# Kernel tuning notes

Hardware: AMD Instinct MI355X
Metric: run time of the kernel (lower is better)

## Reference

```python
import jax, jax.numpy as jnp
import numpy as np

B, C, T = 256, 8, 1000
PATCH, D, SEQ = 20, 192, 400
N_LAYERS, HEADS = 8, 3
DH = D // HEADS  # 64
HID = 4 * D      # 768
NCLS = 7


def fq(x, n=127.0):
    """Symmetric per-tensor int8 fake-quant (brevitas Int8*PerTensorFloat) with STE."""
    s = jnp.max(jnp.abs(x)) / n + 1e-8
    q = jnp.clip(jnp.round(x / s), -n - 1.0, n) * s
    return x + jax.lax.stop_gradient(q - x)


def fq_u(x, n=255.0):
    """Unsigned per-tensor fake-quant for softmax probabilities (integer softmax output)."""
    s = jnp.max(x) / n + 1e-8
    q = jnp.clip(jnp.round(x / s), 0.0, n) * s
    return x + jax.lax.stop_gradient(q - x)


def ln(x, g, b):
    m = x.mean(-1, keepdims=True)
    v = ((x - m) ** 2).mean(-1, keepdims=True)
    return (x - m) * jax.lax.rsqrt(v + 1e-5) * g + b


def setup_inputs() -> dict:
    key = jax.random.key(0)
    ks = jax.random.split(key, 16)
    w = lambda k, shape: (jax.random.normal(k, shape, jnp.float32) * 0.02)
    inp = {
        "x": jax.random.normal(ks[0], (B, 1, C, T), jnp.float32),
        "patch_w": w(ks[1], (D, PATCH)),          # conv kernel [192,1,1,20] squeezed
        "patch_b": jnp.zeros((D,), jnp.float32),
        "ln1_g": jnp.ones((N_LAYERS, D), jnp.float32),
        "ln1_b": jnp.zeros((N_LAYERS, D), jnp.float32),
        "w_qkv": w(ks[2], (N_LAYERS, 3 * D, D)),
        "b_qkv": jnp.zeros((N_LAYERS, 3 * D), jnp.float32),
        "w_o": w(ks[3], (N_LAYERS, D, D)),
        "b_o": jnp.zeros((N_LAYERS, D), jnp.float32),
        "ln2_g": jnp.ones((N_LAYERS, D), jnp.float32),
        "ln2_b": jnp.zeros((N_LAYERS, D), jnp.float32),
        "w1": w(ks[4], (N_LAYERS, HID, D)),
        "b1": jnp.zeros((N_LAYERS, HID), jnp.float32),
        "w2": w(ks[5], (N_LAYERS, D, HID)),
        "b2": jnp.zeros((N_LAYERS, D), jnp.float32),
        "lnf_g": jnp.ones((D,), jnp.float32),
        "lnf_b": jnp.zeros((D,), jnp.float32),
        "clf_w": w(ks[6], (NCLS, D)),
        "clf_b": jnp.zeros((NCLS,), jnp.float32),
    }
    return inp


def reference(x, patch_w, patch_b, ln1_g, ln1_b, w_qkv, b_qkv, w_o, b_o,
              ln2_g, ln2_b, w1, b1, w2, b2, lnf_g, lnf_b, clf_w, clf_b):
    scale = 1.0 / jnp.sqrt(jnp.float32(DH))

    # input quant
    h = fq(x)
    # patch embed: conv (1,20) stride (1,20) == non-overlapping patchify + GEMM
    p = h.reshape(B, C, T // PATCH, PATCH)          # [B,8,50,20]
    emb = jnp.einsum('bcpt,et->bcpe', p, fq(patch_w)) + patch_b
    h = emb.reshape(B, SEQ, D)                      # token = ch*50 + patch, matches conv reshape
    h = fq(h)

    for i in range(N_LAYERS):
        # --- attention ---
        xn = ln(h, ln1_g[i], ln1_b[i])
        qkv = jnp.einsum('bsd,ed->bse', xn, fq(w_qkv[i])) + b_qkv[i]  # [B,S,576]
        q, k, v = jnp.split(qkv, 3, axis=-1)
        q, k, v = fq(q), fq(k), fq(v)
        q = q.reshape(B, SEQ, HEADS, DH).transpose(0, 2, 1, 3)
        k = k.reshape(B, SEQ, HEADS, DH).transpose(0, 2, 1, 3)
        v = v.reshape(B, SEQ, HEADS, DH).transpose(0, 2, 1, 3)
        scores = jnp.einsum('bhsd,bhtd->bhst', q, k) * scale
        scores = fq(scores)
        probs = jax.nn.softmax(scores, axis=-1)
        probs = fq_u(probs)  # integer softmax output (uint8)
        ctx = jnp.einsum('bhst,bhtd->bhsd', probs, v)
        ctx = ctx.transpose(0, 2, 1, 3).reshape(B, SEQ, D)
        ctx = fq(ctx)
        attn = jnp.einsum('bsd,ed->bse', ctx, fq(w_o[i])) + b_o[i]
        attn = fq(attn)
        h = h + attn
        # --- MLP ---
        xn = ln(h, ln2_g[i], ln2_b[i])
        m = jnp.einsum('bsd,hd->bsh', xn, fq(w1[i])) + b1[i]
        m = fq(jax.nn.gelu(m, approximate=False))
        m = jnp.einsum('bsh,dh->bsd', m, fq(w2[i])) + b2[i]
        m = fq(m)
        h = h + m

    h = ln(h, lnf_g, lnf_b)
    pooled = fq(h.mean(axis=1))                      # [B,192]
    logits = jnp.einsum('bd,cd->bc', pooled, fq(clf_w)) + clf_b
    return logits
```

## Files before the change

kernel.cpp:

```cpp
#include <hip/hip_runtime.h>
#include <math.h>


typedef unsigned int u32;
typedef unsigned short u16;
typedef __attribute__((ext_vector_type(4))) int int4v;

#define MFMA_I8(a, b, c) __builtin_amdgcn_mfma_i32_16x16x64_i8((a), (b), (c), 0, 0, 0)

constexpr int NL = 8;
constexpr long ROWS = 102400;
constexpr float LOG2E = 1.44269504088896340736f;

constexpr int SLOT_X = 0, SLOT_PW = 1, SLOT_EMB = 2, SLOT_CLF = 3, SLOT_POOL = 4;
constexpr int N_SLOT_WORDS = 200 * 16;

constexpr long OFF_GM = 3200;
constexpr long OFF_GL = OFF_GM + 307200;
constexpr long OFF_POOL = OFF_GL + 307200;
constexpr long OFF_PWQ = OFF_POOL + 49152;
constexpr long OFF_CLFQ = OFF_PWQ + 3840;
constexpr long OFF_H = OFF_CLFQ + 1344;
constexpr long OFF_A = OFF_H + 19660800;
constexpr long OFF_U = OFF_A + 19660800;

__device__ __forceinline__ float warpMax(float v) {
#pragma unroll
  for (int o = 32; o > 0; o >>= 1) v = fmaxf(v, __shfl_down(v, o));
  return v;
}

__device__ __forceinline__ float read_max16(const u32* sc, int slot) {
  const u32* p = sc + slot * 16;
  u32 m = 0;
#pragma unroll
  for (int i = 0; i < 16; ++i) m = max(m, p[i]);
  return __uint_as_float(m);
}

__device__ __forceinline__ float fqs(float x, float s) {
  return fminf(fmaxf(rintf(x / s), -128.0f), 127.0f) * s;
}

__global__ void k_zero(u32* p, int n) {
  int i = blockIdx.x * blockDim.x + threadIdx.x;
  if (i < n) p[i] = 0u;
}

__global__ __launch_bounds__(256) void k_absmax(const float4* __restrict__ x, long n4,
                                                u32* __restrict__ slot) {
  float m = 0.f;
  for (long i = (long)blockIdx.x * blockDim.x + threadIdx.x; i < n4;
       i += (long)gridDim.x * blockDim.x) {
    float4 v = x[i];
    m = fmaxf(m, fmaxf(fmaxf(fabsf(v.x), fabsf(v.y)), fmaxf(fabsf(v.z), fabsf(v.w))));
  }
  __shared__ float red[4];
  m = warpMax(m);
  int lane = threadIdx.x & 63, w = threadIdx.x >> 6;
  if (lane == 0) red[w] = m;
  __syncthreads();
  if (threadIdx.x == 0) {
    float r = fmaxf(fmaxf(red[0], red[1]), fmaxf(red[2], red[3]));
    atomicMax(slot + (blockIdx.x & 15), __float_as_uint(r));
  }
}

__global__ __launch_bounds__(256) void k_quant4(const float4* __restrict__ in,
                                                float4* __restrict__ out, long n4,
                                                const u32* __restrict__ sc, int slot) {
  float s = read_max16(sc, slot) / 127.0f + 1e-8f;
  for (long i = (long)blockIdx.x * blockDim.x + threadIdx.x; i < n4;
       i += (long)gridDim.x * blockDim.x) {
    float4 v = in[i];
    v.x = fqs(v.x, s); v.y = fqs(v.y, s); v.z = fqs(v.z, s); v.w = fqs(v.w, s);
    out[i] = v;
  }
}

__global__ __launch_bounds__(256) void k_quant_codes(const float4* __restrict__ in,
                                                     u32* __restrict__ out, long n4,
                                                     const u32* __restrict__ sc, int slot) {
  float s = read_max16(sc, slot) / 127.0f + 1e-8f;
  for (long i = (long)blockIdx.x * blockDim.x + threadIdx.x; i < n4;
       i += (long)gridDim.x * blockDim.x) {
    float4 v = in[i];
    int c0 = (int)fminf(fmaxf(rintf(v.x / s), -128.f), 127.f);
    int c1 = (int)fminf(fmaxf(rintf(v.y / s), -128.f), 127.f);
    int c2 = (int)fminf(fmaxf(rintf(v.z / s), -128.f), 127.f);
    int c3 = (int)fminf(fmaxf(rintf(v.w / s), -128.f), 127.f);
    out[i] = (u32)(c0 & 0xff) | ((u32)(c1 & 0xff) << 8) | ((u32)(c2 & 0xff) << 16) |
             ((u32)(c3 & 0xff) << 24);
  }
}

__global__ __launch_bounds__(192) void k_patch(const float* __restrict__ x,
                                               const float* __restrict__ pwq,
                                               const float* __restrict__ pb,
                                               const u32* __restrict__ sc,
                                               float* __restrict__ emb,
                                               u32* __restrict__ embSlot) {
  __shared__ float wsm[3840];
  __shared__ float xq[160];
  __shared__ float red[3];
  const int tid = threadIdx.x;
  const long rowBase = (long)blockIdx.x * 8;
  const float sx = read_max16(sc, SLOT_X) / 127.0f + 1e-8f;
#pragma unroll
  for (int j = 0; j < 5; ++j)
    ((float4*)wsm)[j * 192 + tid] = ((const float4*)pwq)[j * 192 + tid];
  if (tid < 40) {
    float4 v = ((const float4*)(x + rowBase * 20))[tid];
    v.x = fqs(v.x, sx); v.y = fqs(v.y, sx); v.z = fqs(v.z, sx); v.w = fqs(v.w, sx);
    ((float4*)xq)[tid] = v;
  }
  __syncthreads();
  float wreg[20];
#pragma unroll
  for (int k = 0; k < 20; ++k) wreg[k] = wsm[tid * 20 + k];
  const float bias = pb[tid];
  float m = 0.f;
#pragma unroll
  for (int r = 0; r < 8; ++r) {
    float acc = bias;
#pragma unroll
    for (int k = 0; k < 20; ++k) acc += xq[r * 20 + k] * wreg[k];
    emb[(rowBase + r) * 192 + tid] = acc;
    m = fmaxf(m, fabsf(acc));
  }
  m = warpMax(m);
  if ((tid & 63) == 0) red[tid >> 6] = m;
  __syncthreads();
  if (tid == 0)
    atomicMax(embSlot + (blockIdx.x & 15),
              __float_as_uint(fmaxf(fmaxf(red[0], red[1]), red[2])));
}

template <bool RES, bool I16>
__global__ __launch_bounds__(256) void k_resln(float* __restrict__ H,
                                               const float* __restrict__ raw,
                                               const u32* __restrict__ sc, int slotRes,
                                               const float* __restrict__ g,
                                               const float* __restrict__ bta,
                                               signed char* __restrict__ yh,
                                               signed char* __restrict__ yl,
                                               float* __restrict__ sArow,
                                               float* __restrict__ yf, int rows) {
  int w = threadIdx.x >> 6, lane = threadIdx.x & 63;
  long row = (long)blockIdx.x * 4 + w;
  if (row >= rows) return;
  const bool act = lane < 48;
  float4 v = make_float4(0.f, 0.f, 0.f, 0.f);
  if (act) v = ((const float4*)(H + row * 192))[lane];
  if (RES) {
    float sres = read_max16(sc, slotRes) / 127.0f + 1e-8f;
    if (act) {
      float4 r4 = ((const float4*)(raw + row * 192))[lane];
      v.x += fqs(r4.x, sres); v.y += fqs(r4.y, sres);
      v.z += fqs(r4.z, sres); v.w += fqs(r4.w, sres);
      ((float4*)(H + row * 192))[lane] = v;
    }
  }
  float s = v.x + v.y + v.z + v.w;
#pragma unroll
  for (int o = 32; o > 0; o >>= 1) s += __shfl_down(s, o);
  s = __shfl(s, 0);
  float mean = s / 192.0f;
  float d0 = v.x - mean, d1 = v.y - mean, d2 = v.z - mean, d3 = v.w - mean;
  float q = act ? (d0 * d0 + d1 * d1 + d2 * d2 + d3 * d3) : 0.f;
#pragma unroll
  for (int o = 32; o > 0; o >>= 1) q += __shfl_down(q, o);
  q = __shfl(q, 0);
  float rs = 1.0f / sqrtf(q / 192.0f + 1e-5f);
  float4 gv = make_float4(0.f, 0.f, 0.f, 0.f), bv = gv;
  if (act) {
    gv = ((const float4*)g)[lane];
    bv = ((const float4*)bta)[lane];
  }
  float o0 = d0 * rs * gv.x + bv.x;
  float o1 = d1 * rs * gv.y + bv.y;
  float o2 = d2 * rs * gv.z + bv.z;
  float o3 = d3 * rs * gv.w + bv.w;
  if (I16) {
    float rm = act ? fmaxf(fmaxf(fabsf(o0), fabsf(o1)), fmaxf(fabsf(o2), fabsf(o3))) : 0.f;
#pragma unroll
    for (int o = 32; o > 0; o >>= 1) rm = fmaxf(rm, __shfl_down(rm, o));
    rm = __shfl(rm, 0);
    float sA = rm / 32512.0f + 1e-20f;
    float inv = 1.0f / sA;
    if (act) {
      int c0 = (int)rintf(o0 * inv), c1 = (int)rintf(o1 * inv);
      int c2 = (int)rintf(o2 * inv), c3 = (int)rintf(o3 * inv);
      int h0 = (c0 + 128) >> 8, h1 = (c1 + 128) >> 8;
      int h2 = (c2 + 128) >> 8, h3 = (c3 + 128) >> 8;
      int l0 = c0 - (h0 << 8), l1 = c1 - (h1 << 8);
      int l2 = c2 - (h2 << 8), l3 = c3 - (h3 << 8);
      u32 hw = (u32)(h0 & 0xff) | ((u32)(h1 & 0xff) << 8) | ((u32)(h2 & 0xff) << 16) |
               ((u32)(h3 & 0xff) << 24);
      u32 lw = (u32)(l0 & 0xff) | ((u32)(l1 & 0xff) << 8) | ((u32)(l2 & 0xff) << 16) |
               ((u32)(l3 & 0xff) << 24);
      ((u32*)yh)[row * 48 + lane] = hw;
      ((u32*)yl)[row * 48 + lane] = lw;
    }
    if (lane == 0) sArow[row] = sA;
  } else {
    if (act) ((float4*)(yf + row * 192))[lane] = make_float4(o0, o1, o2, o3);
  }
}

__global__ __launch_bounds__(256) void k_wquant(const float4* __restrict__ w,
                                                u32* __restrict__ out, int n4,
                                                const u32* __restrict__ sc, int slot) {
  int i = blockIdx.x * blockDim.x + threadIdx.x;
  if (i >= n4) return;
  float s = read_max16(sc, slot) / 127.0f + 1e-8f;
  float4 v = w[i];
  int c0 = (int)fminf(fmaxf(rintf(v.x / s), -128.f), 127.f);
  int c1 = (int)fminf(fmaxf(rintf(v.y / s), -128.f), 127.f);
  int c2 = (int)fminf(fmaxf(rintf(v.z / s), -128.f), 127.f);
  int c3 = (int)fminf(fmaxf(rintf(v.w / s), -128.f), 127.f);
  out[i] = (u32)(c0 & 0xff) | ((u32)(c1 & 0xff) << 8) | ((u32)(c2 & 0xff) << 16) |
           ((u32)(c3 & 0xff) << 24);
}

template <bool GELU, int OM>
__global__ __launch_bounds__(256) void k_gemm16(
    const signed char* __restrict__ AH, const signed char* __restrict__ AL,
    const float* __restrict__ sArow, const signed char* __restrict__ W8, int slotW,
    const float* __restrict__ bias, signed char* __restrict__ C8, int N, int ncol,
    u32* __restrict__ sc, int slotO, int colsPerSlot) {
  __shared__ __align__(16) signed char Bs[192 * 208];
  __shared__ float red[4];
  const int tid = threadIdx.x;
  const int bid = blockIdx.x;
  const int vid = (bid & 7) * ((int)gridDim.x >> 3) + (bid >> 3);
  const int bx = vid % ncol;
  const long by = vid / ncol;
  const long rowBase = by * 128;
  const int colBase = bx * 192;
  const float sW = read_max16(sc, slotW) / 127.0f + 1e-8f;

  {
    const signed char* wp = W8 + (long)colBase * 192;
#pragma unroll
    for (int it = 0; it < 9; ++it) {
      int idx = it * 256 + tid;
      int row = idx / 12, c = idx % 12;
      int4 v = *(const int4*)(wp + (long)row * 192 + c * 16);
      *(int4*)&Bs[row * 208 + c * 16] = v;
    }
  }

  const int lane = tid & 63, w = tid >> 6;
  const int fr = lane & 15, fk = lane >> 4;
  const int wc0 = w * 48;

  float sOinv = 0.f;
  if (OM == 2) sOinv = 1.0f / (read_max16(sc, slotO + colBase / colsPerSlot) / 127.0f + 1e-8f);
  const float inv_sqrt2 = 0.70710678118654752440f;
  float vmax = 0.f;

  const long abase = (rowBase + fr) * 192 + fk * 16;
  __syncthreads();

#pragma unroll 1
  for (int it = 0; it < 8; ++it) {
    const long ab = abase + (long)it * 16 * 192;
    int4v ahc[3], alc[3];
#pragma unroll
    for (int kk = 0; kk < 3; ++kk) {
      ahc[kk] = *(const int4v*)(AH + ab + kk * 64);
      alc[kk] = *(const int4v*)(AL + ab + kk * 64);
    }
    int4v aH[3], aL[3];
#pragma unroll
    for (int n = 0; n < 3; ++n) {
      aH[n] = (int4v){0, 0, 0, 0};
      aL[n] = (int4v){0, 0, 0, 0};
    }
#pragma unroll
    for (int kk = 0; kk < 3; ++kk) {
#pragma unroll
      for (int n = 0; n < 3; ++n) {
        int4v bfr = *(const int4v*)&Bs[(wc0 + n * 16 + fr) * 208 + kk * 64 + fk * 16];
        aH[n] = MFMA_I8(ahc[kk], bfr, aH[n]);
        aL[n] = MFMA_I8(alc[kk], bfr, aL[n]);
      }
    }
    const long rt = rowBase + it * 16;
    float4 sA4 = *(const float4*)&sArow[rt + fk * 4];
    float sAr[4] = {sA4.x, sA4.y, sA4.z, sA4.w};
#pragma unroll
    for (int n = 0; n < 3; ++n) {
      const int col = colBase + wc0 + n * 16 + fr;
      const float bb = bias[col];
#pragma unroll
      for (int r = 0; r < 4; ++r) {
        const int R = (aH[n][r] << 8) + aL[n][r];
        float val = (float)R * (sAr[r] * sW) + bb;
        if (GELU) val = 0.5f * val * (1.0f + erff(val * inv_sqrt2));
        if (OM == 2) {
          float code = fminf(fmaxf(rintf(val * sOinv), -128.f), 127.f);
          C8[(rt + fk * 4 + r) * N + col] = (signed char)code;
        } else {
          vmax = fmaxf(vmax, fabsf(val));
        }
      }
    }
  }

  if (OM == 1) {
    float m = warpMax(vmax);
    if ((tid & 63) == 0) red[tid >> 6] = m;
    __syncthreads();
    if (tid == 0) {
      float r = fmaxf(fmaxf(red[0], red[1]), fmaxf(red[2], red[3]));
      atomicMax(sc + (slotO + colBase / colsPerSlot) * 16 + ((int)(bx + by) & 15),
                __float_as_uint(r));
    }
  }
}

__global__ __launch_bounds__(256) void k_gemm8(
    const signed char* __restrict__ A8, int slotA, const signed char* __restrict__ W8,
    int slotW, const float* __restrict__ bias, float* __restrict__ C, int N, int K,
    u32* __restrict__ sc, int slotO) {
  __shared__ float red[4];
  const int tid = threadIdx.x;
  const long rowBase = (long)blockIdx.y * 128;
  const int colBase = blockIdx.x * 192;
  const float alpha = (read_max16(sc, slotA) / 127.0f + 1e-8f) *
                      (read_max16(sc, slotW) / 127.0f + 1e-8f);

  const int lane = tid & 63, wv = tid >> 6;
  const int wm = wv >> 1, wn = wv & 1;
  const int fr = lane & 15, fk = lane >> 4;

  int4v acc[4][6];
#pragma unroll
  for (int m = 0; m < 4; ++m)
#pragma unroll
    for (int n = 0; n < 6; ++n) acc[m][n] = (int4v){0, 0, 0, 0};

  const long arow0 = rowBase + wm * 64;
  const int bcol0 = colBase + wn * 96;

  for (int k0 = 0; k0 < K; k0 += 64) {
    const int ko = k0 + fk * 16;
    int4v bfr[6];
#pragma unroll
    for (int n = 0; n < 6; ++n)
      bfr[n] = *(const int4v*)(W8 + (long)(bcol0 + n * 16 + fr) * K + ko);
#pragma unroll
    for (int m = 0; m < 4; ++m) {
      int4v af = *(const int4v*)(A8 + (arow0 + m * 16 + fr) * (long)K + ko);
#pragma unroll
      for (int n = 0; n < 6; ++n) acc[m][n] = MFMA_I8(af, bfr[n], acc[m][n]);
    }
  }

  float vmax = 0.f;
#pragma unroll
  for (int n = 0; n < 6; ++n) {
    const int col = colBase + wn * 96 + n * 16 + fr;
    const float bb = bias[col];
#pragma unroll
    for (int m = 0; m < 4; ++m) {
#pragma unroll
      for (int r = 0; r < 4; ++r) {
        const long row = rowBase + wm * 64 + m * 16 + fk * 4 + r;
        float val = (float)acc[m][n][r] * alpha + bb;
        C[row * N + col] = val;
        vmax = fmaxf(vmax, fabsf(val));
      }
    }
  }
  {
    float m = warpMax(vmax);
    if ((tid & 63) == 0) red[tid >> 6] = m;
    __syncthreads();
    if (tid == 0) {
      float r = fmaxf(fmaxf(red[0], red[1]), fmaxf(red[2], red[3]));
      atomicMax(sc + slotO * 16 + ((blockIdx.x + blockIdx.y) & 15), __float_as_uint(r));
    }
  }
}

__global__ __launch_bounds__(256) void k_vt(const signed char* __restrict__ qkv8,
                                            signed char* __restrict__ vt8,
                                            int* __restrict__ colsum) {
  __shared__ __align__(16) signed char T[64 * 80];
  __shared__ int cs[64];
  const int tid = threadIdx.x;
  const int bh = blockIdx.x, b = bh / 3, hh = bh % 3;
  const signed char* vb = qkv8 + (long)b * 400 * 576 + hh * 64 + 384;
  if (tid < 64) cs[tid] = 0;
  const int d = tid >> 2, seg = tid & 3;
  for (int c0 = 0; c0 < 448; c0 += 64) {
    __syncthreads();
    {
      int trow = tid >> 2, c = tid & 3;
      int4 v = make_int4(0, 0, 0, 0);
      if (c0 + trow < 400) v = *(const int4*)(vb + (long)(c0 + trow) * 576 + c * 16);
      *(int4*)&T[trow * 80 + c * 16] = v;
    }
    __syncthreads();
    int4 outw;
    int ssum = 0;
    u32 pk[4];
#pragma unroll
    for (int j = 0; j < 4; ++j) {
      u32 p = 0;
#pragma unroll
      for (int e = 0; e < 4; ++e) {
        int t = seg * 16 + j * 4 + e;
        int v = (int)T[t * 80 + d];
        ssum += v;
        p |= ((u32)(v & 0xff)) << (8 * e);
      }
      pk[j] = p;
    }
    outw.x = (int)pk[0]; outw.y = (int)pk[1]; outw.z = (int)pk[2]; outw.w = (int)pk[3];
    if (c0 + seg * 16 < 400)
      *(int4*)&vt8[(long)bh * 25600 + d * 400 + c0 + seg * 16] = outw;
    atomicAdd(&cs[d], ssum);
  }
  __syncthreads();
  if (tid < 64) colsum[bh * 64 + tid] = cs[tid];
}

__device__ __forceinline__ void attn_swz(int& tile, int& bh) {
  int bid = blockIdx.x;
  int vid = (bid & 7) * ((int)gridDim.x >> 3) + (bid >> 3);
  tile = vid % 7;
  bh = vid / 7;
}

__global__ __launch_bounds__(256) void k_attn0(const signed char* __restrict__ qkv8,
                                               int* __restrict__ gmInt, u32* __restrict__ sc,
                                               int slotQ, int slotSc) {
  __shared__ float red[4];
  const int tid = threadIdx.x;
  int tile, bh;
  attn_swz(tile, bh);
  const int r0 = tile * 64;
  const int b = bh / 3, hh = bh % 3;
  const signed char* qb = qkv8 + (long)b * 400 * 576 + hh * 64;
  const signed char* kb = qb + 192;
  const float sQ = read_max16(sc, slotQ) / 127.0f + 1e-8f;
  const float sK = read_max16(sc, slotQ + 1) / 127.0f + 1e-8f;
  const float sSc = sQ * sK * 0.125f;

  const int lane = tid & 63, w = tid >> 6, fr = lane & 15, fk = lane >> 4;
  const int qloc = 16 * w + fr;
  const int gq = r0 + qloc;
  const bool qv = gq < 400;
  int4v qf = *(const int4v*)(qb + (long)(r0 + qloc) * 576 + fk * 16);

  int aim = 0;
  int rim = -(1 << 30);
  for (int c0 = 0; c0 < 400; c0 += 128) {
#pragma unroll
    for (int tf = 0; tf < 8; ++tf) {
      int4v kf = *(const int4v*)(kb + (long)(c0 + tf * 16 + fr) * 576 + fk * 16);
      int4v s = MFMA_I8(kf, qf, ((int4v){0, 0, 0, 0}));
      const bool tv = (c0 + tf * 16 + fk * 4) < 400;
      if (tv && qv) {
#pragma unroll
        for (int r = 0; r < 4; ++r) {
          int sv = s[r];
          aim = max(aim, max(sv, -sv));
          rim = max(rim, sv);
        }
      }
    }
  }
  rim = max(rim, __shfl_xor(rim, 16));
  rim = max(rim, __shfl_xor(rim, 32));
  if (fk == 0 && qv) gmInt[(long)bh * 400 + gq] = rim;
  float m = warpMax((float)aim * sSc);
  if (lane == 0) red[w] = m;
  __syncthreads();
  if (tid == 0) {
    float r = fmaxf(fmaxf(red[0], red[1]), fmaxf(red[2], red[3]));
    atomicMax(sc + slotSc * 16 + (blockIdx.x & 15), __float_as_uint(r));
  }
}

__global__ __launch_bounds__(256) void k_attn1(const signed char* __restrict__ qkv8,
                                               float* __restrict__ gm, float* __restrict__ gl,
                                               const int* __restrict__ gmInt,
                                               u32* __restrict__ sc, int slotQ, int slotSc,
                                               int slotPr) {
  __shared__ float red[4];
  const int tid = threadIdx.x;
  int tile, bh;
  attn_swz(tile, bh);
  const int r0 = tile * 64;
  const int b = bh / 3, hh = bh % 3;
  const signed char* qb = qkv8 + (long)b * 400 * 576 + hh * 64;
  const signed char* kb = qb + 192;
  const float sQ = read_max16(sc, slotQ) / 127.0f + 1e-8f;
  const float sK = read_max16(sc, slotQ + 1) / 127.0f + 1e-8f;
  const float sSc = sQ * sK * 0.125f;
  const float sS = read_max16(sc, slotSc) / 127.0f + 1e-8f;
  const float c1 = sSc / sS;
  const float c2 = sS * LOG2E;

  const int lane = tid & 63, w = tid >> 6, fr = lane & 15, fk = lane >> 4;
  const int qloc = 16 * w + fr;
  const int gq = r0 + qloc;
  const int gqc = (gq > 399) ? 399 : gq;
  int4v qf = *(const int4v*)(qb + (long)(r0 + qloc) * 576 + fk * 16);

  const int mint = gmInt[(long)bh * 400 + gqc];
  const float cm = fminf(fmaxf(rintf((float)mint * c1), -128.f), 127.f);

  float sum = 0.f;
  for (int c0 = 0; c0 < 400; c0 += 128) {
#pragma unroll
    for (int tf = 0; tf < 8; ++tf) {
      int4v kf = *(const int4v*)(kb + (long)(c0 + tf * 16 + fr) * 576 + fk * 16);
      int4v s = MFMA_I8(kf, qf, ((int4v){0, 0, 0, 0}));
      if ((c0 + tf * 16 + fk * 4) < 400) {
#pragma unroll
        for (int r = 0; r < 4; ++r) {
          float cf = fminf(fmaxf(rintf((float)s[r] * c1), -128.f), 127.f);
          sum += exp2f((cf - cm) * c2);
        }
      }
    }
  }
  sum += __shfl_xor(sum, 16);
  sum += __shfl_xor(sum, 32);
  float cand = 0.f;
  if (fk == 0 && gq < 400) {
    gm[(long)bh * 400 + gq] = cm;
    gl[(long)bh * 400 + gq] = sum;
    cand = 1.0f / sum;
  }
  float m = warpMax(cand);
  if (lane == 0) red[w] = m;
  __syncthreads();
  if (tid == 0) {
    float r = fmaxf(fmaxf(red[0], red[1]), fmaxf(red[2], red[3]));
    atomicMax(sc + slotPr * 16 + (blockIdx.x & 15), __float_as_uint(r));
  }
}

__global__ __launch_bounds__(256) void k_attn_pv(
    const signed char* __restrict__ qkv8, const signed char* __restrict__ vt8,
    const int* __restrict__ colsumV, float* __restrict__ ctx, const float* __restrict__ gm,
    const float* __restrict__ gl, u32* __restrict__ sc, int slotQ, int slotSc, int slotPr,
    int slotCtx) {
  __shared__ __align__(16) signed char Ps[64 * 144];
  __shared__ int colsV[64];
  __shared__ float red[4];
  const int tid = threadIdx.x;
  int tile, bh;
  attn_swz(tile, bh);
  const int r0 = tile * 64;
  const int b = bh / 3, hh = bh % 3;
  const signed char* qb = qkv8 + (long)b * 400 * 576 + hh * 64;
  const signed char* kb = qb + 192;
  const signed char* vtb = vt8 + (long)bh * 25600;
  const float sQ = read_max16(sc, slotQ) / 127.0f + 1e-8f;
  const float sK = read_max16(sc, slotQ + 1) / 127.0f + 1e-8f;
  const float sV = read_max16(sc, slotQ + 2) / 127.0f + 1e-8f;
  const float sSc = sQ * sK * 0.125f;
  const float sS = read_max16(sc, slotSc) / 127.0f + 1e-8f;
  const float sP = read_max16(sc, slotPr) / 255.0f + 1e-8f;
  const float sPV = sP * sV;
  const float c1 = sSc / sS;
  const float c2 = sS * LOG2E;

  if (tid < 64) colsV[tid] = colsumV[bh * 64 + tid];
  const int lane = tid & 63, w = tid >> 6, fr = lane & 15, fk = lane >> 4;
  const int qloc = 16 * w + fr;
  int4v qf = *(const int4v*)(qb + (long)(r0 + qloc) * 576 + fk * 16);

  int gq = r0 + qloc;
  if (gq > 399) gq = 399;
  const float cm = gm[(long)bh * 400 + gq];
  const float invLsp = 1.0f / (gl[(long)bh * 400 + gq] * sP);

  int4v accd[4];
#pragma unroll
  for (int dt = 0; dt < 4; ++dt) accd[dt] = (int4v){0, 0, 0, 0};
  __syncthreads();

  for (int c0 = 0; c0 < 400; c0 += 128) {
#pragma unroll
    for (int tf = 0; tf < 8; ++tf) {
      int4v kf = *(const int4v*)(kb + (long)(c0 + tf * 16 + fr) * 576 + fk * 16);
      int4v s = MFMA_I8(kf, qf, ((int4v){0, 0, 0, 0}));
      const int tbase = c0 + tf * 16 + fk * 4;
      u32 pack = 0;
      if (tbase < 400) {
#pragma unroll
        for (int r = 0; r < 4; ++r) {
          float cf = fminf(fmaxf(rintf((float)s[r] * c1), -128.f), 127.f);
          float e = exp2f((cf - cm) * c2);
          float pu = fminf(fmaxf(rintf(e * invLsp), 0.f), 255.f);
          int pc = (int)pu - 128;
          pack |= ((u32)(pc & 0xff)) << (8 * r);
        }
      }
      *(u32*)&Ps[qloc * 144 + tf * 16 + fk * 4] = pack;
    }
    __syncthreads();
    int4v pf0 = *(const int4v*)&Ps[qloc * 144 + fk * 16];
    int4v pf1 = *(const int4v*)&Ps[qloc * 144 + 64 + fk * 16];
    const bool v0ok = (c0 + fk * 16) < 400;
    const bool v1ok = (c0 + 64 + fk * 16) < 400;
#pragma unroll
    for (int dt = 0; dt < 4; ++dt) {
      const long vrow = (long)(dt * 16 + fr) * 400;
      int4v vf0 = v0ok ? *(const int4v*)(vtb + vrow + c0 + fk * 16) : (int4v){0, 0, 0, 0};
      int4v vf1 = v1ok ? *(const int4v*)(vtb + vrow + c0 + 64 + fk * 16) : (int4v){0, 0, 0, 0};
      accd[dt] = MFMA_I8(vf0, pf0, accd[dt]);
      accd[dt] = MFMA_I8(vf1, pf1, accd[dt]);
    }
    __syncthreads();
  }
  float vmax = 0.f;
  const int q = r0 + qloc;
  if (q < 400) {
#pragma unroll
    for (int dt = 0; dt < 4; ++dt) {
      const int d0 = dt * 16 + fk * 4;
      float4 o;
      o.x = sPV * (float)(accd[dt][0] + 128 * colsV[d0 + 0]);
      o.y = sPV * (float)(accd[dt][1] + 128 * colsV[d0 + 1]);
      o.z = sPV * (float)(accd[dt][2] + 128 * colsV[d0 + 2]);
      o.w = sPV * (float)(accd[dt][3] + 128 * colsV[d0 + 3]);
      vmax = fmaxf(vmax, fmaxf(fmaxf(fabsf(o.x), fabsf(o.y)), fmaxf(fabsf(o.z), fabsf(o.w))));
      *(float4*)&ctx[(long)(b * 400 + q) * 192 + hh * 64 + d0] = o;
    }
  }
  float m = warpMax(vmax);
  if (lane == 0) red[w] = m;
  __syncthreads();
  if (tid == 0) {
    float r = fmaxf(fmaxf(red[0], red[1]), fmaxf(red[2], red[3]));
    atomicMax(sc + slotCtx * 16 + (blockIdx.x & 15), __float_as_uint(r));
  }
}

__global__ __launch_bounds__(192) void k_pool(const float* __restrict__ xln,
                                              float* __restrict__ pooled,
                                              u32* __restrict__ slot) {
  int b = blockIdx.x, d = threadIdx.x;
  float sum = 0.f;
  for (int s = 0; s < 400; ++s) sum += xln[((long)b * 400 + s) * 192 + d];
  float v = sum / 400.0f;
  pooled[(long)b * 192 + d] = v;
  __shared__ float red[3];
  float m = warpMax(fabsf(v));
  if ((d & 63) == 0) red[d >> 6] = m;
  __syncthreads();
  if (d == 0)
    atomicMax(slot + (b & 15), __float_as_uint(fmaxf(fmaxf(red[0], red[1]), red[2])));
}

__global__ __launch_bounds__(64) void k_logits(const float* __restrict__ pooled,
                                               const float* __restrict__ clfq,
                                               const float* __restrict__ clfb,
                                               const u32* __restrict__ sc,
                                               float* __restrict__ out) {
  int c = blockIdx.x, b = blockIdx.y, lane = threadIdx.x;
  float sp = read_max16(sc, SLOT_POOL) / 127.0f + 1e-8f;
  float acc = 0.f;
#pragma unroll
  for (int j = 0; j < 3; ++j) {
    int d = lane + 64 * j;
    acc += fqs(pooled[(long)b * 192 + d], sp) * clfq[c * 192 + d];
  }
#pragma unroll
  for (int o = 32; o > 0; o >>= 1) acc += __shfl_down(acc, o);
  if (lane == 0) out[b * 7 + c] = acc + clfb[c];
}

static inline int gsz(long n4, long cap) {
  long g = (n4 + 255) / 256;
  return (int)(g < cap ? g : cap);
}

extern "C" void kernel_launch(void* const* d_in, const int* in_sizes, int n_in,
                              void* d_out, int out_size, void* d_ws, size_t ws_size,
                              hipStream_t stream) {
  (void)in_sizes; (void)n_in; (void)out_size; (void)ws_size;

  const float* x = (const float*)d_in[0];
  const float* pw = (const float*)d_in[1];
  const float* pb = (const float*)d_in[2];
  const float* ln1g = (const float*)d_in[3];
  const float* ln1b = (const float*)d_in[4];
  const float* wqkv = (const float*)d_in[5];
  const float* bqkv = (const float*)d_in[6];
  const float* wo = (const float*)d_in[7];
  const float* bo = (const float*)d_in[8];
  const float* ln2g = (const float*)d_in[9];
  const float* ln2b = (const float*)d_in[10];
  const float* w1 = (const float*)d_in[11];
  const float* b1 = (const float*)d_in[12];
  const float* w2 = (const float*)d_in[13];
  const float* b2 = (const float*)d_in[14];
  const float* lnfg = (const float*)d_in[15];
  const float* lnfb = (const float*)d_in[16];
  const float* clfw = (const float*)d_in[17];
  const float* clfb = (const float*)d_in[18];

  float* ws = (float*)d_ws;
  u32* sc = (u32*)d_ws;
  float* GM = ws + OFF_GM;
  int* GMI = (int*)GM;
  float* GL = ws + OFF_GL;
  float* POOL = ws + OFF_POOL;
  float* PWQ = ws + OFF_PWQ;
  float* CLFQ = ws + OFF_CLFQ;
  float* H = ws + OFF_H;

  signed char* RA = (signed char*)(ws + OFF_A);
  signed char* RU = (signed char*)(ws + OFF_U);
  signed char* PLQ_H = RU;
  signed char* PLQ_L = RU + 19660800;
  float* PLQ_S = (float*)(RU + 39321600);
  signed char* QKV8 = RA;
  signed char* VT8 = RA + 58982400;
  float* CTXF = (float*)RU;
  signed char* CTX8 = RA;
  float* WOOUT = (float*)RU;
  signed char* PL2_H = RA;
  signed char* PL2_L = RA + 19660800;
  float* PL2_S = (float*)(RA + 39321600);
  signed char* GELU8 = RU;
  float* W2OUT = (float*)RA;
  float* FINALF = (float*)RU;

  int* COLSUM = (int*)POOL;
  signed char* WQC = (signed char*)POOL;
  signed char* WOC2 = (signed char*)POOL;
  signed char* W1C2 = (signed char*)POOL + 36864;
  signed char* W2C2 = (signed char*)POOL + 36864;
  float* out = (float*)d_out;

  k_zero<<<(N_SLOT_WORDS + 255) / 256, 256, 0, stream>>>(sc, N_SLOT_WORDS);

  auto amax = [&](const float* p, long n, int slot) {
    k_absmax<<<gsz(n / 4, 256), 256, 0, stream>>>((const float4*)p, n / 4, sc + slot * 16);
  };
  amax(pw, 3840, SLOT_PW);
  amax(clfw, 1344, SLOT_CLF);
  amax(x, 2048000, SLOT_X);
  for (int i = 0; i < NL; ++i) {
    int Lb = 16 + i * 16;
    amax(wqkv + (long)i * 110592, 110592, Lb + 0);
    amax(wo + (long)i * 36864, 36864, Lb + 1);
    amax(w1 + (long)i * 147456, 147456, Lb + 2);
    amax(w2 + (long)i * 147456, 147456, Lb + 3);
  }
  k_quant4<<<gsz(960, 256), 256, 0, stream>>>((const float4*)pw, (float4*)PWQ, 960, sc, SLOT_PW);
  k_quant4<<<gsz(336, 256), 256, 0, stream>>>((const float4*)clfw, (float4*)CLFQ, 336, sc,
                                              SLOT_CLF);

  k_patch<<<12800, 192, 0, stream>>>(x, PWQ, pb, sc, (float*)RU, sc + SLOT_EMB * 16);
  k_quant4<<<2048, 256, 0, stream>>>((const float4*)RU, (float4*)H, 19660800 / 4, sc, SLOT_EMB);
  k_resln<false, true><<<(int)(ROWS / 4), 256, 0, stream>>>(
      H, nullptr, sc, 0, ln1g, ln1b, PLQ_H, PLQ_L, PLQ_S, nullptr, (int)ROWS);

  for (int i = 0; i < NL; ++i) {
    int Lb = 16 + i * 16;
    k_wquant<<<108, 256, 0, stream>>>((const float4*)(wqkv + (long)i * 110592), (u32*)WQC,
                                      27648, sc, Lb + 0);
    k_gemm16<false, 1><<<2400, 256, 0, stream>>>(PLQ_H, PLQ_L, PLQ_S, WQC, Lb + 0,
                                                 bqkv + i * 576, nullptr, 576, 3, sc, Lb + 4,
                                                 192);
    k_gemm16<false, 2><<<2400, 256, 0, stream>>>(PLQ_H, PLQ_L, PLQ_S, WQC, Lb + 0,
                                                 bqkv + i * 576, QKV8, 576, 3, sc, Lb + 4,
                                                 192);
    k_vt<<<768, 256, 0, stream>>>(QKV8, VT8, COLSUM);
    k_attn0<<<5376, 256, 0, stream>>>(QKV8, GMI, sc, Lb + 4, Lb + 7);
    k_attn1<<<5376, 256, 0, stream>>>(QKV8, GM, GL, GMI, sc, Lb + 4, Lb + 7, Lb + 8);
    k_attn_pv<<<5376, 256, 0, stream>>>(QKV8, VT8, COLSUM, CTXF, GM, GL, sc, Lb + 4, Lb + 7,
                                        Lb + 8, Lb + 9);
    k_quant_codes<<<2048, 256, 0, stream>>>((const float4*)CTXF, (u32*)CTX8, 19660800 / 4, sc,
                                            Lb + 9);
    k_wquant<<<36, 256, 0, stream>>>((const float4*)(wo + (long)i * 36864), (u32*)WOC2, 9216,
                                     sc, Lb + 1);
    {
      dim3 g(1, 800);
      k_gemm8<<<g, 256, 0, stream>>>(CTX8, Lb + 9, WOC2, Lb + 1, bo + i * 192, WOOUT, 192, 192,
                                     sc, Lb + 10);
    }
    k_resln<true, true><<<(int)(ROWS / 4), 256, 0, stream>>>(
        H, WOOUT, sc, Lb + 10, ln2g + i * 192, ln2b + i * 192, PL2_H, PL2_L, PL2_S, nullptr,
        (int)ROWS);
    k_wquant<<<144, 256, 0, stream>>>((const float4*)(w1 + (long)i * 147456), (u32*)W1C2,
                                      36864, sc, Lb + 2);
    k_gemm16<true, 1><<<3200, 256, 0, stream>>>(PL2_H, PL2_L, PL2_S, W1C2, Lb + 2,
                                                b1 + i * 768, nullptr, 768, 4, sc, Lb + 11,
                                                768);
    k_gemm16<true, 2><<<3200, 256, 0, stream>>>(PL2_H, PL2_L, PL2_S, W1C2, Lb + 2,
                                                b1 + i * 768, GELU8, 768, 4, sc, Lb + 11, 768);
    k_wquant<<<144, 256, 0, stream>>>((const float4*)(w2 + (long)i * 147456), (u32*)W2C2,
                                      36864, sc, Lb + 3);
    {
      dim3 g(1, 800);
      k_gemm8<<<g, 256, 0, stream>>>(GELU8, Lb + 11, W2C2, Lb + 3, b2 + i * 192, W2OUT, 192,
                                     768, sc, Lb + 12);
    }
    if (i < NL - 1) {
      k_resln<true, true><<<(int)(ROWS / 4), 256, 0, stream>>>(
          H, W2OUT, sc, Lb + 12, ln1g + (i + 1) * 192, ln1b + (i + 1) * 192, PLQ_H, PLQ_L,
          PLQ_S, nullptr, (int)ROWS);
    } else {
      k_resln<true, false><<<(int)(ROWS / 4), 256, 0, stream>>>(
          H, W2OUT, sc, Lb + 12, lnfg, lnfb, nullptr, nullptr, nullptr, FINALF, (int)ROWS);
    }
  }

  k_pool<<<256, 192, 0, stream>>>(FINALF, POOL, sc + SLOT_POOL * 16);
  {
    dim3 g(7, 256);
    k_logits<<<g, 64, 0, stream>>>(POOL, CLFQ, clfb, sc, out);
  }
}
```

Before: 6.070 ms.

## Process 128 query rows per attention block; fuse embed quant into first LayerNorm

Attention kernels now handle two 64-row query groups per block (128 rows, 4 tiles per head instead of 7), so each K fragment load feeds two MFMAs and the grid shrinks. In exchange, each block holds more registers and the PV kernel doubles its shared-memory P buffer. The patch-embed kernel stages its output in shared memory and writes it with coalesced float4 stores. The separate embedding quant pass is removed: a new resln mode reads the raw embedding, fake-quantizes it and writes H, dropping one full-tensor pass.

```diff
diff --git a/kernel.cpp b/kernel.cpp
--- a/kernel.cpp
+++ b/kernel.cpp
@@ -102,6 +102,7 @@
                                                u32* __restrict__ embSlot) {
   __shared__ float wsm[3840];
   __shared__ float xq[160];
+  __shared__ float eout[1536];
   __shared__ float red[3];
   const int tid = threadIdx.x;
   const long rowBase = (long)blockIdx.x * 8;
@@ -125,9 +126,13 @@
     float acc = bias;
 #pragma unroll
     for (int k = 0; k < 20; ++k) acc += xq[r * 20 + k] * wreg[k];
-    emb[(rowBase + r) * 192 + tid] = acc;
+    eout[r * 192 + tid] = acc;
     m = fmaxf(m, fabsf(acc));
   }
+  __syncthreads();
+  float4* emb4 = (float4*)(emb + rowBase * 192);
+  emb4[tid] = ((const float4*)eout)[tid];
+  emb4[tid + 192] = ((const float4*)eout)[tid + 192];
   m = warpMax(m);
   if ((tid & 63) == 0) red[tid >> 6] = m;
   __syncthreads();
@@ -136,7 +141,7 @@
               __float_as_uint(fmaxf(fmaxf(red[0], red[1]), red[2])));
 }
 
-template <bool RES, bool I16>
+template <int MODE, bool I16>
 __global__ __launch_bounds__(256) void k_resln(float* __restrict__ H,
                                                const float* __restrict__ raw,
                                                const u32* __restrict__ sc, int slotRes,
@@ -151,8 +156,10 @@
   if (row >= rows) return;
   const bool act = lane < 48;
   float4 v = make_float4(0.f, 0.f, 0.f, 0.f);
-  if (act) v = ((const float4*)(H + row * 192))[lane];
-  if (RES) {
+  if (MODE == 0 || MODE == 1) {
+    if (act) v = ((const float4*)(H + row * 192))[lane];
+  }
+  if (MODE == 1 || MODE == 2) {
     float sres = read_max16(sc, slotRes) / 127.0f + 1e-8f;
     if (act) {
       float4 r4 = ((const float4*)(raw + row * 192))[lane];
@@ -432,8 +439,8 @@
 __device__ __forceinline__ void attn_swz(int& tile, int& bh) {
   int bid = blockIdx.x;
   int vid = (bid & 7) * ((int)gridDim.x >> 3) + (bid >> 3);
-  tile = vid % 7;
-  bh = vid / 7;
+  tile = vid & 3;
+  bh = vid >> 2;
 }
 
 __global__ __launch_bounds__(256) void k_attn0(const signed char* __restrict__ qkv8,
@@ -443,7 +450,7 @@
   const int tid = threadIdx.x;
   int tile, bh;
   attn_swz(tile, bh);
-  const int r0 = tile * 64;
+  const int r0 = tile * 128;
   const int b = bh / 3, hh = bh % 3;
   const signed char* qb = qkv8 + (long)b * 400 * 576 + hh * 64;
   const signed char* kb = qb + 192;
@@ -453,31 +460,45 @@
 
   const int lane = tid & 63, w = tid >> 6, fr = lane & 15, fk = lane >> 4;
   const int qloc = 16 * w + fr;
-  const int gq = r0 + qloc;
-  const bool qv = gq < 400;
-  int4v qf = *(const int4v*)(qb + (long)(r0 + qloc) * 576 + fk * 16);
+  const int gq0 = r0 + qloc, gq1 = gq0 + 64;
+  const bool qv0 = gq0 < 400, qv1 = gq1 < 400;
+  int4v qf0 = *(const int4v*)(qb + (long)gq0 * 576 + fk * 16);
+  int4v qf1 = *(const int4v*)(qb + (long)gq1 * 576 + fk * 16);
 
   int aim = 0;
-  int rim = -(1 << 30);
+  int rim0 = -(1 << 30), rim1 = -(1 << 30);
   for (int c0 = 0; c0 < 400; c0 += 128) {
 #pragma unroll
     for (int tf = 0; tf < 8; ++tf) {
       int4v kf = *(const int4v*)(kb + (long)(c0 + tf * 16 + fr) * 576 + fk * 16);
-      int4v s = MFMA_I8(kf, qf, ((int4v){0, 0, 0, 0}));
+      int4v s0 = MFMA_I8(kf, qf0, ((int4v){0, 0, 0, 0}));
+      int4v s1 = MFMA_I8(kf, qf1, ((int4v){0, 0, 0, 0}));
       const bool tv = (c0 + tf * 16 + fk * 4) < 400;
-      if (tv && qv) {
+      if (tv) {
 #pragma unroll
         for (int r = 0; r < 4; ++r) {
-          int sv = s[r];
-          aim = max(aim, max(sv, -sv));
-          rim = max(rim, sv);
+          if (qv0) {
+            int sv = s0[r];
+            aim = max(aim, max(sv, -sv));
+            rim0 = max(rim0, sv);
+          }
+          if (qv1) {
+            int sv = s1[r];
+            aim = max(aim, max(sv, -sv));
+            rim1 = max(rim1, sv);
+          }
         }
       }
     }
   }
-  rim = max(rim, __shfl_xor(rim, 16));
-  rim = max(rim, __shfl_xor(rim, 32));
-  if (fk == 0 && qv) gmInt[(long)bh * 400 + gq] = rim;
+  rim0 = max(rim0, __shfl_xor(rim0, 16));
+  rim0 = max(rim0, __shfl_xor(rim0, 32));
+  rim1 = max(rim1, __shfl_xor(rim1, 16));
+  rim1 = max(rim1, __shfl_xor(rim1, 32));
+  if (fk == 0) {
+    if (qv0) gmInt[(long)bh * 400 + gq0] = rim0;
+    if (qv1) gmInt[(long)bh * 400 + gq1] = rim1;
+  }
   float m = warpMax((float)aim * sSc);
   if (lane == 0) red[w] = m;
   __syncthreads();
@@ -496,7 +517,7 @@
   const int tid = threadIdx.x;
   int tile, bh;
   attn_swz(tile, bh);
-  const int r0 = tile * 64;
+  const int r0 = tile * 128;
   const int b = bh / 3, hh = bh % 3;
   const signed char* qb = qkv8 + (long)b * 400 * 576 + hh * 64;
   const signed char* kb = qb + 192;
@@ -509,35 +530,49 @@
 
   const int lane = tid & 63, w = tid >> 6, fr = lane & 15, fk = lane >> 4;
   const int qloc = 16 * w + fr;
-  const int gq = r0 + qloc;
-  const int gqc = (gq > 399) ? 399 : gq;
-  int4v qf = *(const int4v*)(qb + (long)(r0 + qloc) * 576 + fk * 16);
-
-  const int mint = gmInt[(long)bh * 400 + gqc];
-  const float cm = fminf(fmaxf(rintf((float)mint * c1), -128.f), 127.f);
-
-  float sum = 0.f;
+  const int gq0 = r0 + qloc, gq1 = gq0 + 64;
+  const int gqc0 = (gq0 > 399) ? 399 : gq0;
+  const int gqc1 = (gq1 > 399) ? 399 : gq1;
+  int4v qf0 = *(const int4v*)(qb + (long)gq0 * 576 + fk * 16);
+  int4v qf1 = *(const int4v*)(qb + (long)gq1 * 576 + fk * 16);
+
+  const float cm0 = fminf(fmaxf(rintf((float)gmInt[(long)bh * 400 + gqc0] * c1), -128.f), 127.f);
+  const float cm1 = fminf(fmaxf(rintf((float)gmInt[(long)bh * 400 + gqc1] * c1), -128.f), 127.f);
+
+  float sum0 = 0.f, sum1 = 0.f;
   for (int c0 = 0; c0 < 400; c0 += 128) {
 #pragma unroll
     for (int tf = 0; tf < 8; ++tf) {
       int4v kf = *(const int4v*)(kb + (long)(c0 + tf * 16 + fr) * 576 + fk * 16);
-      int4v s = MFMA_I8(kf, qf, ((int4v){0, 0, 0, 0}));
+      int4v s0 = MFMA_I8(kf, qf0, ((int4v){0, 0, 0, 0}));
+      int4v s1 = MFMA_I8(kf, qf1, ((int4v){0, 0, 0, 0}));
       if ((c0 + tf * 16 + fk * 4) < 400) {
 #pragma unroll
         for (int r = 0; r < 4; ++r) {
-          float cf = fminf(fmaxf(rintf((float)s[r] * c1), -128.f), 127.f);
-          sum += exp2f((cf - cm) * c2);
+          float cf0 = fminf(fmaxf(rintf((float)s0[r] * c1), -128.f), 127.f);
+          sum0 += exp2f((cf0 - cm0) * c2);
+          float cf1 = fminf(fmaxf(rintf((float)s1[r] * c1), -128.f), 127.f);
+          sum1 += exp2f((cf1 - cm1) * c2);
         }
       }
     }
   }
-  sum += __shfl_xor(sum, 16);
-  sum += __shfl_xor(sum, 32);
+  sum0 += __shfl_xor(sum0, 16);
+  sum0 += __shfl_xor(sum0, 32);
+  sum1 += __shfl_xor(sum1, 16);
+  sum1 += __shfl_xor(sum1, 32);
   float cand = 0.f;
-  if (fk == 0 && gq < 400) {
-    gm[(long)bh * 400 + gq] = cm;
-    gl[(long)bh * 400 + gq] = sum;
-    cand = 1.0f / sum;
+  if (fk == 0) {
+    if (gq0 < 400) {
+      gm[(long)bh * 400 + gq0] = cm0;
+      gl[(long)bh * 400 + gq0] = sum0;
+      cand = fmaxf(cand, 1.0f / sum0);
+    }
+    if (gq1 < 400) {
+      gm[(long)bh * 400 + gq1] = cm1;
+      gl[(long)bh * 400 + gq1] = sum1;
+      cand = fmaxf(cand, 1.0f / sum1);
+    }
   }
   float m = warpMax(cand);
   if (lane == 0) red[w] = m;
@@ -553,13 +588,13 @@
     const int* __restrict__ colsumV, float* __restrict__ ctx, const float* __restrict__ gm,
     const float* __restrict__ gl, u32* __restrict__ sc, int slotQ, int slotSc, int slotPr,
     int slotCtx) {
-  __shared__ __align__(16) signed char Ps[64 * 144];
+  __shared__ __align__(16) signed char Ps[128 * 144];
   __shared__ int colsV[64];
   __shared__ float red[4];
   const int tid = threadIdx.x;
   int tile, bh;
   attn_swz(tile, bh);
-  const int r0 = tile * 64;
+  const int r0 = tile * 128;
   const int b = bh / 3, hh = bh % 3;
   const signed char* qb = qkv8 + (long)b * 400 * 576 + hh * 64;
   const signed char* kb = qb + 192;
@@ -577,40 +612,54 @@
   if (tid < 64) colsV[tid] = colsumV[bh * 64 + tid];
   const int lane = tid & 63, w = tid >> 6, fr = lane & 15, fk = lane >> 4;
   const int qloc = 16 * w + fr;
-  int4v qf = *(const int4v*)(qb + (long)(r0 + qloc) * 576 + fk * 16);
-
-  int gq = r0 + qloc;
-  if (gq > 399) gq = 399;
-  const float cm = gm[(long)bh * 400 + gq];
-  const float invLsp = 1.0f / (gl[(long)bh * 400 + gq] * sP);
-
-  int4v accd[4];
-#pragma unroll
-  for (int dt = 0; dt < 4; ++dt) accd[dt] = (int4v){0, 0, 0, 0};
+  const int gq0r = r0 + qloc, gq1r = gq0r + 64;
+  int4v qf0 = *(const int4v*)(qb + (long)gq0r * 576 + fk * 16);
+  int4v qf1 = *(const int4v*)(qb + (long)gq1r * 576 + fk * 16);
+
+  const int gq0 = (gq0r > 399) ? 399 : gq0r;
+  const int gq1 = (gq1r > 399) ? 399 : gq1r;
+  const float cm0 = gm[(long)bh * 400 + gq0];
+  const float invLsp0 = 1.0f / (gl[(long)bh * 400 + gq0] * sP);
+  const float cm1 = gm[(long)bh * 400 + gq1];
+  const float invLsp1 = 1.0f / (gl[(long)bh * 400 + gq1] * sP);
+
+  int4v accd0[4], accd1[4];
+#pragma unroll
+  for (int dt = 0; dt < 4; ++dt) {
+    accd0[dt] = (int4v){0, 0, 0, 0};
+    accd1[dt] = (int4v){0, 0, 0, 0};
+  }
   __syncthreads();
 
   for (int c0 = 0; c0 < 400; c0 += 128) {
 #pragma unroll
     for (int tf = 0; tf < 8; ++tf) {
       int4v kf = *(const int4v*)(kb + (long)(c0 + tf * 16 + fr) * 576 + fk * 16);
-      int4v s = MFMA_I8(kf, qf, ((int4v){0, 0, 0, 0}));
+      int4v s0 = MFMA_I8(kf, qf0, ((int4v){0, 0, 0, 0}));
+      int4v s1 = MFMA_I8(kf, qf1, ((int4v){0, 0, 0, 0}));
       const int tbase = c0 + tf * 16 + fk * 4;
-      u32 pack = 0;
+      u32 pack0 = 0, pack1 = 0;
       if (tbase < 400) {
 #pragma unroll
         for (int r = 0; r < 4; ++r) {
-          float cf = fminf(fmaxf(rintf((float)s[r] * c1), -128.f), 127.f);
-          float e = exp2f((cf - cm) * c2);
-          float pu = fminf(fmaxf(rintf(e * invLsp), 0.f), 255.f);
-          int pc = (int)pu - 128;
-          pack |= ((u32)(pc & 0xff)) << (8 * r);
+          float cf0 = fminf(fmaxf(rintf((float)s0[r] * c1), -128.f), 127.f);
+          float e0 = exp2f((cf0 - cm0) * c2);
+          float pu0 = fminf(fmaxf(rintf(e0 * invLsp0), 0.f), 255.f);
+          pack0 |= ((u32)(((int)pu0 - 128) & 0xff)) << (8 * r);
+          float cf1 = fminf(fmaxf(rintf((float)s1[r] * c1), -128.f), 127.f);
+          float e1 = exp2f((cf1 - cm1) * c2);
+          float pu1 = fminf(fmaxf(rintf(e1 * invLsp1), 0.f), 255.f);
+          pack1 |= ((u32)(((int)pu1 - 128) & 0xff)) << (8 * r);
         }
       }
-      *(u32*)&Ps[qloc * 144 + tf * 16 + fk * 4] = pack;
+      *(u32*)&Ps[qloc * 144 + tf * 16 + fk * 4] = pack0;
+      *(u32*)&Ps[(qloc + 64) * 144 + tf * 16 + fk * 4] = pack1;
     }
     __syncthreads();
-    int4v pf0 = *(const int4v*)&Ps[qloc * 144 + fk * 16];
-    int4v pf1 = *(const int4v*)&Ps[qloc * 144 + 64 + fk * 16];
+    int4v pf00 = *(const int4v*)&Ps[qloc * 144 + fk * 16];
+    int4v pf01 = *(const int4v*)&Ps[qloc * 144 + 64 + fk * 16];
+    int4v pf10 = *(const int4v*)&Ps[(qloc + 64) * 144 + fk * 16];
+    int4v pf11 = *(const int4v*)&Ps[(qloc + 64) * 144 + 64 + fk * 16];
     const bool v0ok = (c0 + fk * 16) < 400;
     const bool v1ok = (c0 + 64 + fk * 16) < 400;
 #pragma unroll
@@ -618,24 +667,38 @@
       const long vrow = (long)(dt * 16 + fr) * 400;
       int4v vf0 = v0ok ? *(const int4v*)(vtb + vrow + c0 + fk * 16) : (int4v){0, 0, 0, 0};
       int4v vf1 = v1ok ? *(const int4v*)(vtb + vrow + c0 + 64 + fk * 16) : (int4v){0, 0, 0, 0};
-      accd[dt] = MFMA_I8(vf0, pf0, accd[dt]);
-      accd[dt] = MFMA_I8(vf1, pf1, accd[dt]);
+      accd0[dt] = MFMA_I8(vf0, pf00, accd0[dt]);
+      accd0[dt] = MFMA_I8(vf1, pf01, accd0[dt]);
+      accd1[dt] = MFMA_I8(vf0, pf10, accd1[dt]);
+      accd1[dt] = MFMA_I8(vf1, pf11, accd1[dt]);
     }
     __syncthreads();
   }
   float vmax = 0.f;
-  const int q = r0 + qloc;
-  if (q < 400) {
+  if (gq0r < 400) {
 #pragma unroll
     for (int dt = 0; dt < 4; ++dt) {
       const int d0 = dt * 16 + fk * 4;
       float4 o;
-      o.x = sPV * (float)(accd[dt][0] + 128 * colsV[d0 + 0]);
-      o.y = sPV * (float)(accd[dt][1] + 128 * colsV[d0 + 1]);
-      o.z = sPV * (float)(accd[dt][2] + 128 * colsV[d0 + 2]);
-      o.w = sPV * (float)(accd[dt][3] + 128 * colsV[d0 + 3]);
+      o.x = sPV * (float)(accd0[dt][0] + 128 * colsV[d0 + 0]);
+      o.y = sPV * (float)(accd0[dt][1] + 128 * colsV[d0 + 1]);
+      o.z = sPV * (float)(accd0[dt][2] + 128 * colsV[d0 + 2]);
+      o.w = sPV * (float)(accd0[dt][3] + 128 * colsV[d0 + 3]);
       vmax = fmaxf(vmax, fmaxf(fmaxf(fabsf(o.x), fabsf(o.y)), fmaxf(fabsf(o.z), fabsf(o.w))));
-      *(float4*)&ctx[(long)(b * 400 + q) * 192 + hh * 64 + d0] = o;
+      *(float4*)&ctx[(long)(b * 400 + gq0r) * 192 + hh * 64 + d0] = o;
+    }
+  }
+  if (gq1r < 400) {
+#pragma unroll
+    for (int dt = 0; dt < 4; ++dt) {
+      const int d0 = dt * 16 + fk * 4;
+      float4 o;
+      o.x = sPV * (float)(accd1[dt][0] + 128 * colsV[d0 + 0]);
+      o.y = sPV * (float)(accd1[dt][1] + 128 * colsV[d0 + 1]);
+      o.z = sPV * (float)(accd1[dt][2] + 128 * colsV[d0 + 2]);
+      o.w = sPV * (float)(accd1[dt][3] + 128 * colsV[d0 + 3]);
+      vmax = fmaxf(vmax, fmaxf(fmaxf(fabsf(o.x), fabsf(o.y)), fmaxf(fabsf(o.z), fabsf(o.w))));
+      *(float4*)&ctx[(long)(b * 400 + gq1r) * 192 + hh * 64 + d0] = o;
     }
   }
   float m = warpMax(vmax);
@@ -764,10 +827,9 @@
   k_quant4<<<gsz(336, 256), 256, 0, stream>>>((const float4*)clfw, (float4*)CLFQ, 336, sc,
                                               SLOT_CLF);
 
-  k_patch<<<12800, 192, 0, stream>>>(x, PWQ, pb, sc, (float*)RU, sc + SLOT_EMB * 16);
-  k_quant4<<<2048, 256, 0, stream>>>((const float4*)RU, (float4*)H, 19660800 / 4, sc, SLOT_EMB);
-  k_resln<false, true><<<(int)(ROWS / 4), 256, 0, stream>>>(
-      H, nullptr, sc, 0, ln1g, ln1b, PLQ_H, PLQ_L, PLQ_S, nullptr, (int)ROWS);
+  k_patch<<<12800, 192, 0, stream>>>(x, PWQ, pb, sc, (float*)RA, sc + SLOT_EMB * 16);
+  k_resln<2, true><<<(int)(ROWS / 4), 256, 0, stream>>>(
+      H, (const float*)RA, sc, SLOT_EMB, ln1g, ln1b, PLQ_H, PLQ_L, PLQ_S, nullptr, (int)ROWS);
 
   for (int i = 0; i < NL; ++i) {
     int Lb = 16 + i * 16;
@@ -780,9 +842,9 @@
                                                  bqkv + i * 576, QKV8, 576, 3, sc, Lb + 4,
                                                  192);
     k_vt<<<768, 256, 0, stream>>>(QKV8, VT8, COLSUM);
-    k_attn0<<<5376, 256, 0, stream>>>(QKV8, GMI, sc, Lb + 4, Lb + 7);
-    k_attn1<<<5376, 256, 0, stream>>>(QKV8, GM, GL, GMI, sc, Lb + 4, Lb + 7, Lb + 8);
-    k_attn_pv<<<5376, 256, 0, stream>>>(QKV8, VT8, COLSUM, CTXF, GM, GL, sc, Lb + 4, Lb + 7,
+    k_attn0<<<3072, 256, 0, stream>>>(QKV8, GMI, sc, Lb + 4, Lb + 7);
+    k_attn1<<<3072, 256, 0, stream>>>(QKV8, GM, GL, GMI, sc, Lb + 4, Lb + 7, Lb + 8);
+    k_attn_pv<<<3072, 256, 0, stream>>>(QKV8, VT8, COLSUM, CTXF, GM, GL, sc, Lb + 4, Lb + 7,
                                         Lb + 8, Lb + 9);
     k_quant_codes<<<2048, 256, 0, stream>>>((const float4*)CTXF, (u32*)CTX8, 19660800 / 4, sc,
                                             Lb + 9);
@@ -793,7 +855,7 @@
       k_gemm8<<<g, 256, 0, stream>>>(CTX8, Lb + 9, WOC2, Lb + 1, bo + i * 192, WOOUT, 192, 192,
                                      sc, Lb + 10);
     }
-    k_resln<true, true><<<(int)(ROWS / 4), 256, 0, stream>>>(
+    k_resln<1, true><<<(int)(ROWS / 4), 256, 0, stream>>>(
         H, WOOUT, sc, Lb + 10, ln2g + i * 192, ln2b + i * 192, PL2_H, PL2_L, PL2_S, nullptr,
         (int)ROWS);
     k_wquant<<<144, 256, 0, stream>>>((const float4*)(w1 + (long)i * 147456), (u32*)W1C2,
@@ -811,11 +873,11 @@
                                      768, sc, Lb + 12);
     }
     if (i < NL - 1) {
-      k_resln<true, true><<<(int)(ROWS / 4), 256, 0, stream>>>(
+      k_resln<1, true><<<(int)(ROWS / 4), 256, 0, stream>>>(
           H, W2OUT, sc, Lb + 12, ln1g + (i + 1) * 192, ln1b + (i + 1) * 192, PLQ_H, PLQ_L,
           PLQ_S, nullptr, (int)ROWS);
     } else {
-      k_resln<true, false><<<(int)(ROWS / 4), 256, 0, stream>>>(
+      k_resln<1, false><<<(int)(ROWS / 4), 256, 0, stream>>>(
           H, W2OUT, sc, Lb + 12, lnfg, lnfb, nullptr, nullptr, nullptr, FINALF, (int)ROWS);
     }
   }
```

Result: faster. 5.787 ms (-4.7%).
